# Kernel optimization log

Hardware: AMD Instinct MI355X
Metric: run time of the kernel (lower is better)

The kernel has to match this reference:

```python
import jax, jax.numpy as jnp
import numpy as np

S = 1024      # seq_len
H = 768       # hidden_size
L = 50        # num_labels
E = 65536     # num_edges
SW = 10       # span_width


def setup_inputs() -> dict:
    key = jax.random.key(0)
    ks = jax.random.split(key, 10)
    hidden_states = jax.random.normal(ks[0], (1, S, H), jnp.float32)
    src = jax.random.randint(ks[1], (E,), 0, S)
    tgt = jax.random.randint(ks[2], (E,), 0, S)
    lbl = jax.random.randint(ks[3], (E,), 0, L)
    edges = jnp.stack([src, tgt, lbl], axis=-1)[None].astype(jnp.int32)  # [1,E,3]
    gcn_W = (jax.random.normal(ks[4], (L, H, H)) * 0.02).astype(jnp.float32)
    gcn_b = jnp.zeros((L, H), jnp.float32)
    attn_w = (jax.random.normal(ks[5], (H,)) * 0.02).astype(jnp.float32)
    attn_b = jnp.zeros((), jnp.float32)
    D = 3 * H
    ms_W1 = (jax.random.normal(ks[6], (D, D)) * 0.02).astype(jnp.float32)
    ms_b1 = jnp.zeros((D,), jnp.float32)
    ms_W2 = (jax.random.normal(ks[7], (D,)) * 0.02).astype(jnp.float32)
    ms_b2 = jnp.zeros((), jnp.float32)
    ant_W = (jax.random.normal(ks[8], (2 * D,)) * 0.02).astype(jnp.float32)
    ant_b = jnp.zeros((), jnp.float32)
    # candidate spans exactly as generate_candidate_spans with span_width=SW
    starts, ends = [], []
    for i in range(S):
        for j in range(i + 1, min(i + SW, S)):
            starts.append(i)
            ends.append(j)
    span_starts = jnp.asarray(np.array(starts, dtype=np.int32))
    span_ends = jnp.asarray(np.array(ends, dtype=np.int32))
    topk = int(S * 0.4)  # seq_lens*0.4 with all-ones attention mask
    return {
        'hidden_states': hidden_states, 'edges': edges,
        'gcn_W': gcn_W, 'gcn_b': gcn_b,
        'attn_w': attn_w, 'attn_b': attn_b,
        'ms_W1': ms_W1, 'ms_b1': ms_b1, 'ms_W2': ms_W2, 'ms_b2': ms_b2,
        'ant_W': ant_W, 'ant_b': ant_b,
        'span_starts': span_starts, 'span_ends': span_ends, 'topk': topk,
    }


def reference(hidden_states, edges, gcn_W, gcn_b, attn_w, attn_b,
              ms_W1, ms_b1, ms_W2, ms_b2, ant_W, ant_b,
              span_starts, span_ends, topk):
    B, Sq, Hd = hidden_states.shape  # B == 1
    nl = gcn_W.shape[0]
    x = hidden_states[0]  # [S,H]

    # ---- GCNLayer: per-label linear + scatter-add + degree norm + relu ----
    src = edges[0, :, 0]
    tgt = edges[0, :, 1]
    lbl = edges[0, :, 2]
    # aggregate source embeddings by (target,label): equivalent to applying
    # W_l per edge then index_add, since the transform is linear per label.
    seg = tgt * nl + lbl                               # [E]
    src_emb = x[src]                                   # [E,H]  gather
    agg = jax.ops.segment_sum(src_emb, seg, num_segments=Sq * nl)
    agg = agg.reshape(Sq, nl, Hd)                      # [S,L,H]
    cnt = jax.ops.segment_sum(jnp.ones_like(seg, jnp.float32), seg,
                              num_segments=Sq * nl).reshape(Sq, nl)
    out = jnp.einsum('slh,lhd->sd', agg, gcn_W) + cnt @ gcn_b  # [S,H]
    degree = jnp.clip(cnt.sum(axis=1), 1.0)[:, None]
    gcn_out = jax.nn.relu(out / degree)

    # combine_strategy == 'add'
    emb = x + gcn_out                                  # [S,H]

    # ---- SpanRepresentation: attention pooling over each span ----
    offs = jnp.arange(SW)                              # span length <= SW
    pos = span_starts[:, None] + offs                  # [N,SW]
    valid = pos <= span_ends[:, None]
    pos_c = jnp.minimum(pos, Sq - 1)
    win = emb[pos_c]                                   # [N,SW,H] gather
    scores = win @ attn_w + attn_b                     # [N,SW]
    scores = jnp.where(valid, scores, -1e9)
    aw = jax.nn.softmax(scores, axis=1)
    attn_out = jnp.einsum('nw,nwh->nh', aw, win)       # [N,H]
    span_vec = jnp.concatenate([emb[span_starts], emb[span_ends], attn_out],
                               axis=-1)                # [N,3H]

    # ---- MentionScorer ----
    hdn = jax.nn.relu(span_vec @ ms_W1 + ms_b1)
    mention_scores = hdn @ ms_W2 + ms_b2               # [N]

    # ---- prune_spans: top-k ----
    topk_scores, topk_idx = jax.lax.top_k(mention_scores, topk)
    pruned = span_vec[topk_idx]                        # [k,3H]

    # ---- antecedent scores: linear over concat pair == sum of two matvecs ----
    D = span_vec.shape[-1]
    s_i = pruned @ ant_W[:D]                           # [k]
    s_j = pruned @ ant_W[D:]                           # [k]
    ant_scores = s_i[:, None] + s_j[None, :] + ant_b   # [k,k]
    # triu mask (antecedent must strictly precede the mention)
    k = pruned.shape[0]
    triu = jnp.triu(jnp.ones((k, k), bool), k=0)
    ant_scores = jnp.where(triu, -1e4, ant_scores)
    dummy = jnp.zeros((k, 1), ant_scores.dtype)
    ant_scores_with_dummy = jnp.concatenate([dummy, ant_scores], axis=1)  # [k,k+1]
    return ant_scores_with_dummy
```

## Files before the change

kernel.cpp:

```cpp
#include <hip/hip_runtime.h>
#include <stdint.h>

typedef __attribute__((ext_vector_type(4))) float f32x4;
typedef __attribute__((ext_vector_type(4))) int i32x4;
typedef __attribute__((ext_vector_type(8))) int i32x8;

#define S_TOK 1024
#define H_DIM 768
#define NLBL  50
#define NEDGE 65536
#define NSEG  (S_TOK * NLBL)
#define NSPAN 9171
#define MPAD  9216
#define DDIM  2304
#define KTOP  409

__device__ __forceinline__ unsigned short f32_to_bf16u(float f) {
  unsigned u = __float_as_uint(f);
  u += 0x7fffu + ((u >> 16) & 1u);
  return (unsigned short)(u >> 16);
}
__device__ __forceinline__ float bf16u_to_f32(unsigned short h) {
  return __uint_as_float(((unsigned)h) << 16);
}
__device__ __forceinline__ unsigned short pack_fp8x2(float a, float b) {
  return (unsigned short)(__builtin_amdgcn_cvt_pk_fp8_f32(a, b, 0, false) & 0xffff);
}
__device__ __forceinline__ unsigned pack_fp8x4(float a, float b, float c, float d) {
  int v = __builtin_amdgcn_cvt_pk_fp8_f32(a, b, 0, false);
  v = __builtin_amdgcn_cvt_pk_fp8_f32(c, d, v, true);
  return (unsigned)v;
}
__device__ __forceinline__ unsigned char pack_fp8x1(float a) {
  return (unsigned char)(__builtin_amdgcn_cvt_pk_fp8_f32(a, a, 0, false) & 0xff);
}

__device__ __forceinline__ void gl_lds16(const void* g, void* l) {
  __builtin_amdgcn_global_load_lds((const __attribute__((address_space(1))) void*)g,
                                   (__attribute__((address_space(3))) void*)l, 16, 0, 0);
}

__global__ __launch_bounds__(256) void convert_fp8(
    const float* __restrict__ in, unsigned* __restrict__ out, int nquads) {
  int i = blockIdx.x * 256 + threadIdx.x;
  if (i >= nquads) return;
  float4 v = ((const float4*)in)[i];
  out[i] = pack_fp8x4(v.x, v.y, v.z, v.w);
}

__global__ __launch_bounds__(256) void transpose_fp8_b(
    const float* __restrict__ in, unsigned char* __restrict__ out, int R, int C) {
  __shared__ float tile[32][33];
  size_t boff = (size_t)blockIdx.z * R * C;
  int tx = threadIdx.x & 31, ty = threadIdx.x >> 5;
  int c0 = blockIdx.x * 32, r0 = blockIdx.y * 32;
#pragma unroll
  for (int i = 0; i < 4; i++)
    tile[ty + 8 * i][tx] = in[boff + (size_t)(r0 + ty + 8 * i) * C + c0 + tx];
  __syncthreads();
#pragma unroll
  for (int i = 0; i < 4; i++)
    out[boff + (size_t)(c0 + ty + 8 * i) * R + r0 + tx] = pack_fp8x1(tile[tx][ty + 8 * i]);
}

__global__ void edge_count2(const int* __restrict__ edges, int* __restrict__ seg_count,
                            int* __restrict__ tgt_count) {
  int e = blockIdx.x * 256 + threadIdx.x;
  if (e >= NEDGE) return;
  int tgt = edges[e * 3 + 1], lbl = edges[e * 3 + 2];
  atomicAdd(&seg_count[tgt * NLBL + lbl], 1);
  atomicAdd(&tgt_count[tgt], 1);
}

__global__ __launch_bounds__(1024) void scan_t(
    const int* __restrict__ cnt, int* __restrict__ offs) {
  __shared__ int part[1024];
  int t = threadIdx.x;
  int c = cnt[t];
  part[t] = c;
  __syncthreads();
  for (int o = 1; o < 1024; o <<= 1) {
    int v = part[t];
    int u = (t >= o) ? part[t - o] : 0;
    __syncthreads();
    part[t] = v + u;
    __syncthreads();
  }
  offs[t] = part[t] - c;
  if (t == 1023) offs[1024] = part[t];
}

__global__ void edge_scatter_t(const int* __restrict__ edges, const int* __restrict__ tgt_off,
                               int* __restrict__ cursor, int* __restrict__ sorted_row) {
  int e = blockIdx.x * 256 + threadIdx.x;
  if (e >= NEDGE) return;
  int src = edges[e * 3], tgt = edges[e * 3 + 1], lbl = edges[e * 3 + 2];
  int pos = tgt_off[tgt] + atomicAdd(&cursor[tgt], 1);
  sorted_row[pos] = lbl * S_TOK + src;
}

template <int EPI>
__global__ __launch_bounds__(256) void gemm_fp8(
    const unsigned char* __restrict__ A, const unsigned char* __restrict__ B,
    unsigned char* __restrict__ Y, float* __restrict__ C,
    const float* __restrict__ b1, const float* __restrict__ w2,
    int M, int Nn, int Kb, int mb, size_t strideB, size_t strideY) {
  __shared__ unsigned char As[128 * 128];
  __shared__ unsigned char Bs[128 * 128];
  int im = blockIdx.x % mb, in_ = blockIdx.x / mb;
  int m0 = im * 128, n0 = in_ * 128;
  const unsigned char* Bl = B + (size_t)blockIdx.y * strideB;

  int t = threadIdx.x;
  int wave = t >> 6, lane = t & 63;
  int wr = wave >> 1, wc = wave & 1;
  int quad = lane >> 4, l15 = lane & 15;
  int lrow = lane >> 3;
  int lk = ((lane & 7) ^ lrow) << 4;

  f32x4 acc[4][4];
  f32x4 zero = {0.f, 0.f, 0.f, 0.f};
#pragma unroll
  for (int mi = 0; mi < 4; mi++)
#pragma unroll
    for (int ni = 0; ni < 4; ni++) acc[mi][ni] = zero;

  for (int kt = 0; kt < Kb; kt += 128) {
#pragma unroll
    for (int i = 0; i < 4; i++) {
      int c = i * 4 + wave;
      int r = c * 8 + lrow;
      gl_lds16(A + (size_t)(m0 + r) * Kb + kt + lk, &As[c * 1024]);
      gl_lds16(Bl + (size_t)(n0 + r) * Kb + kt + lk, &Bs[c * 1024]);
    }
    __syncthreads();
    i32x8 af[4], bg[4];
#pragma unroll
    for (int mi = 0; mi < 4; mi++) {
      int r = wr * 64 + mi * 16 + l15;
      int base = r * 128;
      i32x4 lo = *(const i32x4*)&As[base + (((2 * quad) ^ (r & 7)) << 4)];
      i32x4 hi = *(const i32x4*)&As[base + (((2 * quad + 1) ^ (r & 7)) << 4)];
      af[mi] = __builtin_shufflevector(lo, hi, 0, 1, 2, 3, 4, 5, 6, 7);
    }
#pragma unroll
    for (int ni = 0; ni < 4; ni++) {
      int r = wc * 64 + ni * 16 + l15;
      int base = r * 128;
      i32x4 lo = *(const i32x4*)&Bs[base + (((2 * quad) ^ (r & 7)) << 4)];
      i32x4 hi = *(const i32x4*)&Bs[base + (((2 * quad + 1) ^ (r & 7)) << 4)];
      bg[ni] = __builtin_shufflevector(lo, hi, 0, 1, 2, 3, 4, 5, 6, 7);
    }
#pragma unroll
    for (int mi = 0; mi < 4; mi++)
#pragma unroll
      for (int ni = 0; ni < 4; ni++)
        acc[mi][ni] = __builtin_amdgcn_mfma_scale_f32_16x16x128_f8f6f4(
            af[mi], bg[ni], acc[mi][ni], 0, 0, 0, 0x7f7f7f7f, 0, 0x7f7f7f7f);
    __syncthreads();
  }

  if (EPI == 0) {
    unsigned char* Yl = Y + (size_t)blockIdx.y * strideY;
#pragma unroll
    for (int mi = 0; mi < 4; mi++)
#pragma unroll
      for (int ni = 0; ni < 4; ni++)
#pragma unroll
        for (int r = 0; r < 4; r++)
          As[(wr * 64 + mi * 16 + quad * 4 + r) * 128 + wc * 64 + ni * 16 + l15] =
              pack_fp8x1(acc[mi][ni][r]);
    __syncthreads();
#pragma unroll
    for (int i = 0; i < 4; i++) {
      int idx = t + i * 256;
      int row = idx >> 3, off2 = (idx & 7) << 4;
      *(i32x4*)(Yl + (size_t)(m0 + row) * Nn + n0 + off2) = *(const i32x4*)&As[row * 128 + off2];
    }
  } else {
    float b1v[4], w2v[4];
#pragma unroll
    for (int ni = 0; ni < 4; ni++) {
      int gn = n0 + wc * 64 + ni * 16 + l15;
      b1v[ni] = b1[gn];
      w2v[ni] = w2[gn];
    }
#pragma unroll
    for (int mi = 0; mi < 4; mi++) {
      int gm = m0 + wr * 64 + mi * 16 + quad * 4;
      float part[4] = {0.f, 0.f, 0.f, 0.f};
#pragma unroll
      for (int ni = 0; ni < 4; ni++)
#pragma unroll
        for (int r = 0; r < 4; r++)
          part[r] += fmaxf(acc[mi][ni][r] + b1v[ni], 0.f) * w2v[ni];
#pragma unroll
      for (int o = 1; o < 16; o <<= 1)
#pragma unroll
        for (int r = 0; r < 4; r++) part[r] += __shfl_xor(part[r], o, 64);
      if (l15 == 0) {
#pragma unroll
        for (int r = 0; r < 4; r++)
          if (gm + r < M) atomicAdd(&C[gm + r], part[r]);
      }
    }
  }
}

__global__ __launch_bounds__(192) void gather_emb_kernel(
    const float* __restrict__ x, const unsigned char* __restrict__ Y,
    const int* __restrict__ tgt_off, const int* __restrict__ sorted_row,
    const int* __restrict__ seg_count, const float* __restrict__ gcn_b,
    float* __restrict__ emb) {
  int s = blockIdx.x;
  int t = threadIdx.x;
  int b = tgt_off[s], e = tgt_off[s + 1];
  float a0 = 0.f, a1 = 0.f, a2 = 0.f, a3 = 0.f;
  int p = b;
  for (; p + 1 < e; p += 2) {
    const unsigned* r0 = (const unsigned*)(Y + (size_t)sorted_row[p] * H_DIM);
    const unsigned* r1 = (const unsigned*)(Y + (size_t)sorted_row[p + 1] * H_DIM);
    unsigned w0 = r0[t], w1 = r1[t];
    a0 += __builtin_amdgcn_cvt_f32_fp8(w0, 0) + __builtin_amdgcn_cvt_f32_fp8(w1, 0);
    a1 += __builtin_amdgcn_cvt_f32_fp8(w0, 1) + __builtin_amdgcn_cvt_f32_fp8(w1, 1);
    a2 += __builtin_amdgcn_cvt_f32_fp8(w0, 2) + __builtin_amdgcn_cvt_f32_fp8(w1, 2);
    a3 += __builtin_amdgcn_cvt_f32_fp8(w0, 3) + __builtin_amdgcn_cvt_f32_fp8(w1, 3);
  }
  if (p < e) {
    unsigned w0 = ((const unsigned*)(Y + (size_t)sorted_row[p] * H_DIM))[t];
    a0 += __builtin_amdgcn_cvt_f32_fp8(w0, 0);
    a1 += __builtin_amdgcn_cvt_f32_fp8(w0, 1);
    a2 += __builtin_amdgcn_cvt_f32_fp8(w0, 2);
    a3 += __builtin_amdgcn_cvt_f32_fp8(w0, 3);
  }
  float deg = 0.f, b0 = 0.f, b1 = 0.f, b2 = 0.f, b3 = 0.f;
#pragma unroll 5
  for (int l = 0; l < NLBL; l++) {
    float c = (float)seg_count[s * NLBL + l];
    deg += c;
    float4 g = ((const float4*)(gcn_b + l * H_DIM))[t];
    b0 += c * g.x; b1 += c * g.y; b2 += c * g.z; b3 += c * g.w;
  }
  float dinv = 1.f / fmaxf(deg, 1.f);
  float4 xe = ((const float4*)(x + (size_t)s * H_DIM))[t];
  float4 o;
  o.x = xe.x + fmaxf((a0 + b0) * dinv, 0.f);
  o.y = xe.y + fmaxf((a1 + b1) * dinv, 0.f);
  o.z = xe.z + fmaxf((a2 + b2) * dinv, 0.f);
  o.w = xe.w + fmaxf((a3 + b3) * dinv, 0.f);
  ((float4*)(emb + (size_t)s * H_DIM))[t] = o;
}

__global__ __launch_bounds__(256) void span_kernel(
    const float* __restrict__ emb, const float* __restrict__ attn_w,
    unsigned char* __restrict__ spanv) {
  int i = blockIdx.x;
  int nsp = 1023 - i; if (nsp > 9) nsp = 9;
  if (nsp <= 0) return;
  int nrow = nsp + 1;
  __shared__ float rows[10][768];
  __shared__ float dsh[10];
  int t = threadIdx.x;
  for (int idx = t; idx < nrow * 384; idx += 256) {
    int r = idx / 384, c2 = idx % 384;
    float2 v = ((const float2*)(emb + (size_t)(i + r) * H_DIM))[c2];
    rows[r][c2 * 2] = v.x; rows[r][c2 * 2 + 1] = v.y;
  }
  __syncthreads();
  int wave = t >> 6, lane = t & 63;
  for (int w = wave; w < nrow; w += 4) {
    float p = 0.f;
#pragma unroll
    for (int q = 0; q < 12; q++) p += rows[w][lane + 64 * q] * attn_w[lane + 64 * q];
#pragma unroll
    for (int o = 1; o < 64; o <<= 1) p += __shfl_xor(p, o, 64);
    if (lane == 0) dsh[w] = p;
  }
  __syncthreads();
  float d[10], ex[10];
  float mx = -1e30f;
  for (int w = 0; w < nrow; w++) { d[w] = dsh[w]; mx = fmaxf(mx, d[w]); }
  for (int w = 0; w < nrow; w++) ex[w] = __expf(d[w] - mx);
  bool has2 = (t < 128);
  float n00 = ex[0] * rows[0][2 * t], n01 = ex[0] * rows[0][2 * t + 1];
  float n10 = 0.f, n11 = 0.f;
  if (has2) { n10 = ex[0] * rows[0][2 * t + 512]; n11 = ex[0] * rows[0][2 * t + 513]; }
  float S = ex[0];
  int dd = i - 1014;
  int base = 9 * i - (dd > 0 ? dd * (dd - 1) / 2 : 0);
  unsigned short s0a = pack_fp8x2(rows[0][2 * t], rows[0][2 * t + 1]);
  unsigned short s0b = has2 ? pack_fp8x2(rows[0][2 * t + 512], rows[0][2 * t + 513]) : (unsigned short)0;
  for (int k = 1; k <= nsp; k++) {
    S += ex[k];
    n00 += ex[k] * rows[k][2 * t]; n01 += ex[k] * rows[k][2 * t + 1];
    if (has2) { n10 += ex[k] * rows[k][2 * t + 512]; n11 += ex[k] * rows[k][2 * t + 513]; }
    float inv = 1.f / S;
    unsigned short* out16 = (unsigned short*)(spanv + (size_t)(base + k - 1) * DDIM);
    out16[t] = s0a;
    out16[384 + t] = pack_fp8x2(rows[k][2 * t], rows[k][2 * t + 1]);
    out16[768 + t] = pack_fp8x2(n00 * inv, n01 * inv);
    if (has2) {
      out16[t + 256] = s0b;
      out16[384 + t + 256] = pack_fp8x2(rows[k][2 * t + 512], rows[k][2 * t + 513]);
      out16[768 + t + 256] = pack_fp8x2(n10 * inv, n11 * inv);
    }
  }
}

__device__ __forceinline__ unsigned score_key(float s) {
  unsigned b = __float_as_uint(s);
  return (b & 0x80000000u) ? ~b : (b | 0x80000000u);
}

__global__ __launch_bounds__(1024) void topk_kernel(
    const float* __restrict__ scores, int* __restrict__ topk_idx) {
  __shared__ unsigned skeys[NSPAN];
  __shared__ int hist[16 * 256];
  __shared__ int hsum[256];
  __shared__ unsigned sh_prefix;
  __shared__ int sh_remaining, sh_cnt;
  __shared__ unsigned long long keys[512];
  int t = threadIdx.x;
  int wv = t >> 6;
  for (int i = t; i < NSPAN; i += 1024) skeys[i] = score_key(scores[i]);
  unsigned prefix = 0;
  int remaining = KTOP;
  for (int p = 3; p >= 0; p--) {
    for (int b = t; b < 16 * 256; b += 1024) hist[b] = 0;
    __syncthreads();
    for (int i = t; i < NSPAN; i += 1024) {
      unsigned u = skeys[i];
      bool ok = (p == 3) ? true : ((u >> ((p + 1) * 8)) == prefix);
      if (ok) atomicAdd(&hist[wv * 256 + ((u >> (p * 8)) & 0xff)], 1);
    }
    __syncthreads();
    if (t < 256) {
      int s = 0;
#pragma unroll
      for (int w = 0; w < 16; w++) s += hist[w * 256 + t];
      hsum[t] = s;
    }
    __syncthreads();
    if (t == 0) {
      int rem = remaining;
      int b = 255;
      for (;; b--) {
        int c = hsum[b];
        if (c >= rem) break;
        rem -= c;
      }
      sh_prefix = (prefix << 8) | (unsigned)b;
      sh_remaining = rem;
    }
    __syncthreads();
    prefix = sh_prefix;
    remaining = sh_remaining;
    __syncthreads();
  }
  unsigned kth = prefix;
  if (t == 0) sh_cnt = 0;
  __syncthreads();
  for (int i = t; i < NSPAN; i += 1024) {
    unsigned u = skeys[i];
    if (u >= kth) {
      int pos = atomicAdd(&sh_cnt, 1);
      if (pos < 512) keys[pos] = (((unsigned long long)(~u)) << 32) | (unsigned)i;
    }
  }
  __syncthreads();
  int cnt = sh_cnt < 512 ? sh_cnt : 512;
  for (int i = t; i < 512; i += 1024)
    if (i >= cnt) keys[i] = ~0ull;
  __syncthreads();
  for (int ksz = 2; ksz <= 512; ksz <<= 1)
    for (int j = ksz >> 1; j > 0; j >>= 1) {
      if (t < 512) {
        int ixj = t ^ j;
        if (ixj > t) {
          unsigned long long a = keys[t], b = keys[ixj];
          bool up = ((t & ksz) == 0);
          if (up ? (a > b) : (a < b)) { keys[t] = b; keys[ixj] = a; }
        }
      }
      __syncthreads();
    }
  for (int i = t; i < KTOP; i += 1024) topk_idx[i] = (int)(keys[i] & 0xffffffffu);
}

__global__ __launch_bounds__(256) void sij_kernel(
    const unsigned char* __restrict__ spanv, const int* __restrict__ topk_idx,
    const float* __restrict__ antW, float* __restrict__ s_i, float* __restrict__ s_j) {
  int r = blockIdx.x;
  int idx = topk_idx[r];
  const unsigned* row32 = (const unsigned*)(spanv + (size_t)idx * DDIM);
  int t = threadIdx.x, lane = t & 63, wave = t >> 6;
  float pi = 0.f, pj = 0.f;
  for (int q = t; q < DDIM / 4; q += 256) {
    unsigned w = row32[q];
    float v0 = __builtin_amdgcn_cvt_f32_fp8(w, 0);
    float v1 = __builtin_amdgcn_cvt_f32_fp8(w, 1);
    float v2 = __builtin_amdgcn_cvt_f32_fp8(w, 2);
    float v3 = __builtin_amdgcn_cvt_f32_fp8(w, 3);
    const float* ai = antW + q * 4;
    const float* aj = antW + DDIM + q * 4;
    pi += v0 * ai[0] + v1 * ai[1] + v2 * ai[2] + v3 * ai[3];
    pj += v0 * aj[0] + v1 * aj[1] + v2 * aj[2] + v3 * aj[3];
  }
  for (int o = 32; o; o >>= 1) {
    pi += __shfl_down(pi, o, 64);
    pj += __shfl_down(pj, o, 64);
  }
  __shared__ float ri[4], rj[4];
  if (lane == 0) { ri[wave] = pi; rj[wave] = pj; }
  __syncthreads();
  if (t == 0) {
    s_i[r] = ri[0] + ri[1] + ri[2] + ri[3];
    s_j[r] = rj[0] + rj[1] + rj[2] + rj[3];
  }
}

__global__ void out_kernel(const float* __restrict__ s_i, const float* __restrict__ s_j,
                           const float* __restrict__ ant_b, float* __restrict__ out) {
  int idx = blockIdx.x * 256 + threadIdx.x;
  if (idx >= KTOP * (KTOP + 1)) return;
  int i = idx / (KTOP + 1), c = idx % (KTOP + 1);
  float v;
  if (c == 0) v = 0.f;
  else {
    int j = c - 1;
    v = (j >= i) ? -10000.f : (s_i[i] + s_j[j] + ant_b[0]);
  }
  out[idx] = v;
}

extern "C" void kernel_launch(void* const* d_in, const int* in_sizes, int n_in,
                              void* d_out, int out_size, void* d_ws, size_t ws_size,
                              hipStream_t stream) {
  const float* x      = (const float*)d_in[0];
  const int*   edges  = (const int*)d_in[1];
  const float* gcn_W  = (const float*)d_in[2];
  const float* gcn_b  = (const float*)d_in[3];
  const float* attn_w = (const float*)d_in[4];
  const float* ms_W1  = (const float*)d_in[6];
  const float* ms_b1  = (const float*)d_in[7];
  const float* ms_W2  = (const float*)d_in[8];
  const float* ant_W  = (const float*)d_in[10];
  const float* ant_b  = (const float*)d_in[11];

  size_t off = 0;
  char* wsb = (char*)d_ws;
  auto alloc = [&](size_t bytes) -> void* {
    void* p = wsb + off;
    off += (bytes + 255) & ~(size_t)255;
    return p;
  };
  unsigned char* Y     = (unsigned char*)alloc((size_t)NLBL * S_TOK * H_DIM);
  unsigned char* WtB   = (unsigned char*)alloc((size_t)NLBL * H_DIM * H_DIM);
  unsigned char* Wt2   = (unsigned char*)alloc((size_t)DDIM * DDIM);
  unsigned char* spanv = (unsigned char*)alloc((size_t)MPAD * DDIM);
  unsigned char* Xb    = (unsigned char*)alloc((size_t)S_TOK * H_DIM);
  int* seg_count  = (int*)alloc(NSEG * 4);
  int* tgt_count  = (int*)alloc(S_TOK * 4);
  int* cursor     = (int*)alloc(S_TOK * 4);
  float* scores   = (float*)alloc(MPAD * 4);
  size_t zero_bytes = (char*)(scores + MPAD) - (char*)seg_count;
  int* tgt_off    = (int*)alloc((S_TOK + 4) * 4);
  int* sorted_row = (int*)alloc(NEDGE * 4);
  float* emb    = (float*)alloc((size_t)S_TOK * H_DIM * 4);
  int* topk_idx = (int*)alloc(512 * 4);
  float* s_i    = (float*)alloc(512 * 4);
  float* s_j    = (float*)alloc(512 * 4);
  (void)ws_size; (void)in_sizes; (void)n_in; (void)out_size;

  hipMemsetAsync(seg_count, 0, zero_bytes, stream);

  dim3 b256(256);
  convert_fp8<<<(S_TOK * H_DIM / 4 + 255) / 256, b256, 0, stream>>>(x, (unsigned*)Xb,
                                                                    S_TOK * H_DIM / 4);
  transpose_fp8_b<<<dim3(H_DIM / 32, H_DIM / 32, NLBL), b256, 0, stream>>>(gcn_W, WtB, H_DIM, H_DIM);
  transpose_fp8_b<<<dim3(DDIM / 32, DDIM / 32, 1), b256, 0, stream>>>(ms_W1, Wt2, DDIM, DDIM);
  edge_count2<<<NEDGE / 256, b256, 0, stream>>>(edges, seg_count, tgt_count);
  scan_t<<<1, 1024, 0, stream>>>(tgt_count, tgt_off);
  edge_scatter_t<<<NEDGE / 256, b256, 0, stream>>>(edges, tgt_off, cursor, sorted_row);
  gemm_fp8<0><<<dim3(48, NLBL), b256, 0, stream>>>(
      Xb, WtB, Y, nullptr, nullptr, nullptr,
      S_TOK, H_DIM, H_DIM, 8, (size_t)H_DIM * H_DIM, (size_t)S_TOK * H_DIM);
  gather_emb_kernel<<<S_TOK, dim3(192), 0, stream>>>(x, Y, tgt_off, sorted_row, seg_count, gcn_b, emb);
  span_kernel<<<S_TOK, b256, 0, stream>>>(emb, attn_w, spanv);
  gemm_fp8<1><<<dim3(72 * 18, 1), b256, 0, stream>>>(
      spanv, Wt2, nullptr, scores, ms_b1, ms_W2,
      NSPAN, DDIM, DDIM, 72, 0, 0);
  topk_kernel<<<1, 1024, 0, stream>>>(scores, topk_idx);
  sij_kernel<<<KTOP, b256, 0, stream>>>(spanv, topk_idx, ant_W, s_i, s_j);
  out_kernel<<<(KTOP * (KTOP + 1) + 255) / 256, b256, 0, stream>>>(s_i, s_j, ant_b, (float*)d_out);
}
```

Baseline: 451.5 us.

## Stage edge indices in LDS, widen span-vector stores, parallelize top-k bucket search

The gather kernel now preloads each token's sorted edge row indices into shared memory, so the inner loop no longer does a dependent global index load per edge. The span attention kernel switches from 16-bit fp8x2 stores over 256 threads to 32-bit fp8x4 stores over 192 threads. The top-k radix select replaces the serial single-thread bucket scan with a parallel suffix-sum over the 256 histogram bins. These cut per-edge latency, store instruction count and serial work, at the cost of extra barriers in the suffix scan.

```diff
diff --git a/kernel.cpp b/kernel.cpp
--- a/kernel.cpp
+++ b/kernel.cpp
@@ -15,11 +15,6 @@
 #define DDIM  2304
 #define KTOP  409
 
-__device__ __forceinline__ unsigned short f32_to_bf16u(float f) {
-  unsigned u = __float_as_uint(f);
-  u += 0x7fffu + ((u >> 16) & 1u);
-  return (unsigned short)(u >> 16);
-}
 __device__ __forceinline__ float bf16u_to_f32(unsigned short h) {
   return __uint_as_float(((unsigned)h) << 16);
 }
@@ -212,22 +207,28 @@
     const int* __restrict__ tgt_off, const int* __restrict__ sorted_row,
     const int* __restrict__ seg_count, const float* __restrict__ gcn_b,
     float* __restrict__ emb) {
+  __shared__ int ed[512];
   int s = blockIdx.x;
   int t = threadIdx.x;
   int b = tgt_off[s], e = tgt_off[s + 1];
+  int n = e - b;
+  for (int i = t; i < n && i < 512; i += 192) ed[i] = sorted_row[b + i];
+  __syncthreads();
   float a0 = 0.f, a1 = 0.f, a2 = 0.f, a3 = 0.f;
-  int p = b;
-  for (; p + 1 < e; p += 2) {
-    const unsigned* r0 = (const unsigned*)(Y + (size_t)sorted_row[p] * H_DIM);
-    const unsigned* r1 = (const unsigned*)(Y + (size_t)sorted_row[p + 1] * H_DIM);
-    unsigned w0 = r0[t], w1 = r1[t];
+  int p = 0;
+  for (; p + 1 < n; p += 2) {
+    int i0 = (p < 512) ? ed[p] : sorted_row[b + p];
+    int i1 = (p + 1 < 512) ? ed[p + 1] : sorted_row[b + p + 1];
+    unsigned w0 = ((const unsigned*)(Y + (size_t)i0 * H_DIM))[t];
+    unsigned w1 = ((const unsigned*)(Y + (size_t)i1 * H_DIM))[t];
     a0 += __builtin_amdgcn_cvt_f32_fp8(w0, 0) + __builtin_amdgcn_cvt_f32_fp8(w1, 0);
     a1 += __builtin_amdgcn_cvt_f32_fp8(w0, 1) + __builtin_amdgcn_cvt_f32_fp8(w1, 1);
     a2 += __builtin_amdgcn_cvt_f32_fp8(w0, 2) + __builtin_amdgcn_cvt_f32_fp8(w1, 2);
     a3 += __builtin_amdgcn_cvt_f32_fp8(w0, 3) + __builtin_amdgcn_cvt_f32_fp8(w1, 3);
   }
-  if (p < e) {
-    unsigned w0 = ((const unsigned*)(Y + (size_t)sorted_row[p] * H_DIM))[t];
+  if (p < n) {
+    int i0 = (p < 512) ? ed[p] : sorted_row[b + p];
+    unsigned w0 = ((const unsigned*)(Y + (size_t)i0 * H_DIM))[t];
     a0 += __builtin_amdgcn_cvt_f32_fp8(w0, 0);
     a1 += __builtin_amdgcn_cvt_f32_fp8(w0, 1);
     a2 += __builtin_amdgcn_cvt_f32_fp8(w0, 2);
@@ -281,28 +282,29 @@
   float mx = -1e30f;
   for (int w = 0; w < nrow; w++) { d[w] = dsh[w]; mx = fmaxf(mx, d[w]); }
   for (int w = 0; w < nrow; w++) ex[w] = __expf(d[w] - mx);
-  bool has2 = (t < 128);
-  float n00 = ex[0] * rows[0][2 * t], n01 = ex[0] * rows[0][2 * t + 1];
-  float n10 = 0.f, n11 = 0.f;
-  if (has2) { n10 = ex[0] * rows[0][2 * t + 512]; n11 = ex[0] * rows[0][2 * t + 513]; }
+  bool act = (t < 192);
+  float n0 = 0.f, n1 = 0.f, n2 = 0.f, n3 = 0.f;
+  unsigned s0w = 0;
+  if (act) {
+    float ra = rows[0][4 * t], rb = rows[0][4 * t + 1];
+    float rc = rows[0][4 * t + 2], rd = rows[0][4 * t + 3];
+    s0w = pack_fp8x4(ra, rb, rc, rd);
+    n0 = ex[0] * ra; n1 = ex[0] * rb; n2 = ex[0] * rc; n3 = ex[0] * rd;
+  }
   float S = ex[0];
   int dd = i - 1014;
   int base = 9 * i - (dd > 0 ? dd * (dd - 1) / 2 : 0);
-  unsigned short s0a = pack_fp8x2(rows[0][2 * t], rows[0][2 * t + 1]);
-  unsigned short s0b = has2 ? pack_fp8x2(rows[0][2 * t + 512], rows[0][2 * t + 513]) : (unsigned short)0;
   for (int k = 1; k <= nsp; k++) {
     S += ex[k];
-    n00 += ex[k] * rows[k][2 * t]; n01 += ex[k] * rows[k][2 * t + 1];
-    if (has2) { n10 += ex[k] * rows[k][2 * t + 512]; n11 += ex[k] * rows[k][2 * t + 513]; }
-    float inv = 1.f / S;
-    unsigned short* out16 = (unsigned short*)(spanv + (size_t)(base + k - 1) * DDIM);
-    out16[t] = s0a;
-    out16[384 + t] = pack_fp8x2(rows[k][2 * t], rows[k][2 * t + 1]);
-    out16[768 + t] = pack_fp8x2(n00 * inv, n01 * inv);
-    if (has2) {
-      out16[t + 256] = s0b;
-      out16[384 + t + 256] = pack_fp8x2(rows[k][2 * t + 512], rows[k][2 * t + 513]);
-      out16[768 + t + 256] = pack_fp8x2(n10 * inv, n11 * inv);
+    if (act) {
+      float ra = rows[k][4 * t], rb = rows[k][4 * t + 1];
+      float rc = rows[k][4 * t + 2], rd = rows[k][4 * t + 3];
+      n0 += ex[k] * ra; n1 += ex[k] * rb; n2 += ex[k] * rc; n3 += ex[k] * rd;
+      float inv = 1.f / S;
+      unsigned* o32 = (unsigned*)(spanv + (size_t)(base + k - 1) * DDIM);
+      o32[t]       = s0w;
+      o32[192 + t] = pack_fp8x4(ra, rb, rc, rd);
+      o32[384 + t] = pack_fp8x4(n0 * inv, n1 * inv, n2 * inv, n3 * inv);
     }
   }
 }
@@ -341,16 +343,20 @@
       hsum[t] = s;
     }
     __syncthreads();
-    if (t == 0) {
-      int rem = remaining;
-      int b = 255;
-      for (;; b--) {
-        int c = hsum[b];
-        if (c >= rem) break;
-        rem -= c;
+    for (int o = 1; o < 256; o <<= 1) {
+      int v = 0, u = 0;
+      if (t < 256) { v = hsum[t]; u = (t + o < 256) ? hsum[t + o] : 0; }
+      __syncthreads();
+      if (t < 256) hsum[t] = v + u;
+      __syncthreads();
+    }
+    if (t < 256) {
+      int Sb = hsum[t];
+      int Sb1 = (t < 255) ? hsum[t + 1] : 0;
+      if (Sb >= remaining && Sb1 < remaining) {
+        sh_prefix = (prefix << 8) | (unsigned)t;
+        sh_remaining = remaining - Sb1;
       }
-      sh_prefix = (prefix << 8) | (unsigned)b;
-      sh_remaining = rem;
     }
     __syncthreads();
     prefix = sh_prefix;
```

New measurement: 424.8 us (median of 2 runs). 5.9% less time.
